# Optimization experiments

Hardware: AMD Instinct MI355X
Metric: run time of the kernel (lower is better)

Reference implementation:

```python
import jax, jax.numpy as jnp
import numpy as np

V, E = 4096, 8192
HV, HE, OUT = 256, 128, 256
EPS = 1e-6


def _one_hot_incidence(idx, n_rows, n_cols):
    # incidence matrix M[v, e] = 1 if idx[e] == v
    return jnp.zeros((n_rows, n_cols), jnp.float32).at[idx, jnp.arange(n_cols)].set(1.0)


def setup_inputs() -> dict:
    key = jax.random.key(0)
    ks = jax.random.split(key, 12)
    # edge endpoints: first V source indices cover every vertex -> positive degrees
    u_idx = jnp.concatenate([jnp.arange(V), jax.random.randint(ks[0], (E - V,), 0, V)])
    v_idx = jax.random.randint(ks[1], (E,), 0, V)
    vew1 = _one_hot_incidence(u_idx, V, E)
    vew2 = _one_hot_incidence(v_idx, V, E)
    hv_ftr = jax.random.normal(ks[2], (V, HV), jnp.float32)
    he_ftr = jax.random.normal(ks[3], (E, HE), jnp.float32)
    s = lambda d: 1.0 / np.sqrt(d)
    w_att = jax.random.normal(ks[4], (HV + HE + HV, 1), jnp.float32) * s(HV + HE + HV)
    b_att = jnp.zeros((1,), jnp.float32)
    w_gcn = jax.random.normal(ks[5], (HV, HV), jnp.float32) * s(HV)
    b_gcn = jnp.zeros((HV,), jnp.float32)
    w1 = jax.random.normal(ks[6], (2 * HV, HV), jnp.float32) * s(2 * HV)
    b1 = jnp.zeros((HV,), jnp.float32)
    w2 = jax.random.normal(ks[7], (HV, OUT), jnp.float32) * s(HV)
    b2 = jnp.zeros((OUT,), jnp.float32)
    return dict(hv_ftr=hv_ftr, he_ftr=he_ftr, vew1=vew1, vew2=vew2,
                w_att=w_att, b_att=b_att, w_gcn=w_gcn, b_gcn=b_gcn,
                w1=w1, b1=b1, w2=w2, b2=b2)


def reference(hv_ftr, he_ftr, vew1, vew2, w_att, b_att, w_gcn, b_gcn, w1, b1, w2, b2):
    vew_u = jnp.concatenate([vew1, vew2], axis=1)  # [V, 2E]
    vew_v = jnp.concatenate([vew2, vew1], axis=1)  # [V, 2E]
    hv_u = vew_u.T @ hv_ftr                         # [2E, HV] gather of source feats
    hv_v = vew_v.T @ hv_ftr                         # [2E, HV] gather of target feats
    he2 = jnp.concatenate([he_ftr, he_ftr], axis=0)  # [2E, HE]
    uev = jnp.concatenate([hv_u, he2, hv_v], axis=1)  # [2E, 2HV+HE]
    edge_w = jax.nn.sigmoid(uev @ w_att + b_att).reshape(-1)  # [2E]
    adj = vew_u @ (vew_v * edge_w[None, :]).T       # [V, V]
    # normalize_adj_rc: D_r^{-1/2} A D_c^{-1/2}
    d_r = jax.lax.rsqrt(jnp.maximum(adj.sum(axis=1), EPS))
    d_c = jax.lax.rsqrt(jnp.maximum(adj.sum(axis=0), EPS))
    adj_n = adj * d_r[:, None] * d_c[None, :]
    # GCN(hv_dim->hv_dim, tanh): propagate linear-transformed features
    hidden = jnp.tanh(adj_n @ (hv_ftr @ w_gcn + b_gcn))  # [V, HV]
    # MLP remap: [hv, hidden] -> hidden_dim HV -> OUT (dropout off at inference)
    h = jnp.concatenate([hv_ftr, hidden], axis=1)   # [V, 2HV]
    h = jax.nn.leaky_relu(h @ w1 + b1)
    return h @ w2 + b2                               # [V, OUT]
```

## Files before the change

kernel.cpp:

```cpp
#include <hip/hip_runtime.h>
#include <hip/hip_bf16.h>
#include <math.h>

#define V 4096
#define E 8192
#define HV 256
#define HE 128
#define OUT_DIM 256
#define EPS 1e-6f

#define G_GEMM1 256
#define G_PROJ  512
#define G_ZERO  64
#define G_IDX   8192
#define G_TOTAL (G_GEMM1 + G_PROJ + G_ZERO + G_IDX)

typedef __attribute__((ext_vector_type(8))) short short8;
typedef __attribute__((ext_vector_type(4))) float f32x4;

__device__ __forceinline__ unsigned short f2bf(float f) {
    __hip_bfloat16 h = __float2bfloat16(f);
    return *(unsigned short*)&h;
}

__device__ __forceinline__ short8 cvt8(float4 a, float4 b) {
    short8 r;
    r[0] = f2bf(a.x); r[1] = f2bf(a.y); r[2] = f2bf(a.z); r[3] = f2bf(a.w);
    r[4] = f2bf(b.x); r[5] = f2bf(b.y); r[6] = f2bf(b.z); r[7] = f2bf(b.w);
    return r;
}

template <int ACT>
__device__ __forceinline__ void gemm_body(const float* __restrict__ A0,
                                          const float* __restrict__ A1,
                                          int KSEG, int NSEG,
                                          const float* __restrict__ B,
                                          const float* __restrict__ bias,
                                          float* __restrict__ Cout,
                                          int N, int bm, int bn) {
    __shared__ __align__(16) unsigned short As[64 * 40];
    __shared__ __align__(16) unsigned short Bs[64 * 40];
    const int tid  = threadIdx.x;
    const int lane = tid & 63;
    const int w    = tid >> 6;
    const int wm   = w >> 1, wn = w & 1;
    const int Ktot = KSEG * NSEG;

    const int sr  = tid >> 2;
    const int sc8 = (tid & 3) * 8;
    const int kb  = tid & 31;
    const int bc0 = (tid >> 5) * 8;
    const int fr  = lane & 15;
    const int kc  = (lane >> 4) * 8;

    f32x4 acc[2][2] = {};

    for (int k0 = 0; k0 < Ktot; k0 += 32) {
        const float* Asrc = (k0 >= KSEG) ? A1 : A0;
        int kk = (k0 >= KSEG) ? (k0 - KSEG) : k0;
        const float* ap = &Asrc[(size_t)(bm + sr) * KSEG + kk + sc8];
        float4 a0 = *(const float4*)ap;
        float4 a1 = *(const float4*)(ap + 4);
        const float* bp = &B[(size_t)(k0 + kb) * N + bn + bc0];
        float4 b0 = *(const float4*)bp;
        float4 b1 = *(const float4*)(bp + 4);
        *(short8*)&As[sr * 40 + sc8] = cvt8(a0, a1);
        unsigned short bw[8];
        bw[0] = f2bf(b0.x); bw[1] = f2bf(b0.y); bw[2] = f2bf(b0.z); bw[3] = f2bf(b0.w);
        bw[4] = f2bf(b1.x); bw[5] = f2bf(b1.y); bw[6] = f2bf(b1.z); bw[7] = f2bf(b1.w);
        #pragma unroll
        for (int j = 0; j < 8; ++j) Bs[(bc0 + j) * 40 + kb] = bw[j];
        __syncthreads();

        short8 bfr[2];
        bfr[0] = *(const short8*)&Bs[(wn * 32 + 0 * 16 + fr) * 40 + kc];
        bfr[1] = *(const short8*)&Bs[(wn * 32 + 1 * 16 + fr) * 40 + kc];
        #pragma unroll
        for (int ms = 0; ms < 2; ++ms) {
            short8 af = *(const short8*)&As[(wm * 32 + ms * 16 + fr) * 40 + kc];
            acc[ms][0] = __builtin_amdgcn_mfma_f32_16x16x32_bf16(af, bfr[0], acc[ms][0], 0, 0, 0);
            acc[ms][1] = __builtin_amdgcn_mfma_f32_16x16x32_bf16(af, bfr[1], acc[ms][1], 0, 0, 0);
        }
        __syncthreads();
    }

    #pragma unroll
    for (int ms = 0; ms < 2; ++ms) {
        #pragma unroll
        for (int ns = 0; ns < 2; ++ns) {
            int col = bn + wn * 32 + ns * 16 + fr;
            float bv = bias ? bias[col] : 0.0f;
            #pragma unroll
            for (int r = 0; r < 4; ++r) {
                int row = bm + wm * 32 + ms * 16 + ((lane >> 4) << 2) + r;
                float v = acc[ms][ns][r] + bv;
                if (ACT == 1) v = (v > 0.0f) ? v : 0.01f * v;
                Cout[(size_t)row * N + col] = v;
            }
        }
    }
}

template <int ACT>
__global__ __launch_bounds__(256) void gemm_kernel(const float* __restrict__ A0,
                                                   const float* __restrict__ A1,
                                                   int KSEG, int NSEG,
                                                   const float* __restrict__ B,
                                                   const float* __restrict__ bias,
                                                   float* __restrict__ C, int N) {
    gemm_body<ACT>(A0, A1, KSEG, NSEG, B, bias, C, N, blockIdx.y * 64, blockIdx.x * 64);
}

__global__ __launch_bounds__(256) void mega_kernel(
    const float* __restrict__ hv, const float* __restrict__ he,
    const float4* __restrict__ vew1, const float4* __restrict__ vew2,
    const float* __restrict__ watt,
    const float* __restrict__ wgcn, const float* __restrict__ bgcn,
    int* __restrict__ iu, int* __restrict__ iv,
    float* __restrict__ pu, float* __restrict__ pv, float* __restrict__ pe,
    float4* __restrict__ zbase, int zn4,
    float* __restrict__ X) {
    const int b = blockIdx.x;
    const int tid = threadIdx.x;

    if (b < G_GEMM1) {
        gemm_body<0>(hv, hv, HV, 1, wgcn, bgcn, X, HV, (b >> 2) * 64, (b & 3) * 64);
    } else if (b < G_GEMM1 + G_PROJ) {
        const int lane = tid & 63;
        for (int r = (b - G_GEMM1) * 4 + (tid >> 6); r < V + E; r += G_PROJ * 4) {
            if (r < V) {
                float4 x  = *(const float4*)(hv + (size_t)r * HV + lane * 4);
                float4 wu = *(const float4*)(watt + lane * 4);
                float4 wv = *(const float4*)(watt + HV + HE + lane * 4);
                float su = x.x * wu.x + x.y * wu.y + x.z * wu.z + x.w * wu.w;
                float sv = x.x * wv.x + x.y * wv.y + x.z * wv.z + x.w * wv.w;
                #pragma unroll
                for (int o = 32; o > 0; o >>= 1) {
                    su += __shfl_down(su, o);
                    sv += __shfl_down(sv, o);
                }
                if (lane == 0) { pu[r] = su; pv[r] = sv; }
            } else {
                int e = r - V;
                float2 x = *(const float2*)(he + (size_t)e * HE + lane * 2);
                float2 w = *(const float2*)(watt + HV + lane * 2);
                float s = x.x * w.x + x.y * w.y;
                #pragma unroll
                for (int o = 32; o > 0; o >>= 1) s += __shfl_down(s, o);
                if (lane == 0) pe[e] = s;
            }
        }
    } else if (b < G_GEMM1 + G_PROJ + G_ZERO) {
        float4 z = {0.0f, 0.0f, 0.0f, 0.0f};
        for (int i = (b - G_GEMM1 - G_PROJ) * 256 + tid; i < zn4; i += G_ZERO * 256)
            zbase[i] = z;
    } else {
        int ib = b - (G_GEMM1 + G_PROJ + G_ZERO);
        const float4* m = (ib < G_IDX / 2) ? vew1 : vew2;
        int* o = (ib < G_IDX / 2) ? iu : iv;
        ib &= (G_IDX / 2 - 1);
        size_t base = (size_t)ib * 2048 + tid;
        #pragma unroll
        for (int it = 0; it < 8; ++it) {
            size_t i = base + (size_t)it * 256;
            float4 x = m[i];
            if (x.x + x.y + x.z + x.w > 0.5f) {
                int v  = (int)(i >> 11);
                int c4 = ((int)i & 2047) << 2;
                if (x.x > 0.5f) o[c4 + 0] = v;
                if (x.y > 0.5f) o[c4 + 1] = v;
                if (x.z > 0.5f) o[c4 + 2] = v;
                if (x.w > 0.5f) o[c4 + 3] = v;
            }
        }
    }
}

__global__ __launch_bounds__(256) void edge_kernel(const int* __restrict__ iu,
                                                   const int* __restrict__ iv,
                                                   const float* __restrict__ pu,
                                                   const float* __restrict__ pv,
                                                   const float* __restrict__ pe,
                                                   const float* __restrict__ batt,
                                                   float* __restrict__ ew,
                                                   float* __restrict__ dr,
                                                   float* __restrict__ dc) {
    int e2 = blockIdx.x * blockDim.x + threadIdx.x;
    if (e2 >= 2 * E) return;
    int e  = (e2 < E) ? e2 : e2 - E;
    int uu = (e2 < E) ? iu[e] : iv[e];
    int vv = (e2 < E) ? iv[e] : iu[e];
    float x = pu[uu] + pe[e] + pv[vv] + batt[0];
    float w = 1.0f / (1.0f + expf(-x));
    ew[e2] = w;
    atomicAdd(dr + uu, w);
    atomicAdd(dc + vv, w);
}

__global__ __launch_bounds__(64) void scatter_kernel(const int* __restrict__ iu,
                                                     const int* __restrict__ iv,
                                                     const float* __restrict__ ew,
                                                     const float* __restrict__ dc,
                                                     const float* __restrict__ X,
                                                     float* __restrict__ acc) {
    int e2 = blockIdx.x;
    int t  = threadIdx.x;
    int e  = (e2 < E) ? e2 : e2 - E;
    int uu = (e2 < E) ? iu[e] : iv[e];
    int vv = (e2 < E) ? iv[e] : iu[e];
    float coef = ew[e2] * rsqrtf(fmaxf(dc[vv], EPS));
    float4 x = *(const float4*)(X + (size_t)vv * HV + t * 4);
    float* dst = acc + (size_t)uu * HV + t * 4;
    atomicAdd(dst + 0, coef * x.x);
    atomicAdd(dst + 1, coef * x.y);
    atomicAdd(dst + 2, coef * x.z);
    atomicAdd(dst + 3, coef * x.w);
}

__global__ __launch_bounds__(256) void finish_kernel(const float* __restrict__ dr,
                                                     float4* __restrict__ acc) {
    int i = blockIdx.x * 256 + threadIdx.x;
    int row = i >> 6;
    float s = rsqrtf(fmaxf(dr[row], EPS));
    float4 x = acc[i];
    x.x = tanhf(s * x.x); x.y = tanhf(s * x.y);
    x.z = tanhf(s * x.z); x.w = tanhf(s * x.w);
    acc[i] = x;
}

extern "C" void kernel_launch(void* const* d_in, const int* in_sizes, int n_in,
                              void* d_out, int out_size, void* d_ws, size_t ws_size,
                              hipStream_t stream) {
    const float* hv   = (const float*)d_in[0];
    const float* he   = (const float*)d_in[1];
    const float* vew1 = (const float*)d_in[2];
    const float* vew2 = (const float*)d_in[3];
    const float* watt = (const float*)d_in[4];
    const float* batt = (const float*)d_in[5];
    const float* wgcn = (const float*)d_in[6];
    const float* bgcn = (const float*)d_in[7];
    const float* w1   = (const float*)d_in[8];
    const float* b1   = (const float*)d_in[9];
    const float* w2   = (const float*)d_in[10];
    const float* b2   = (const float*)d_in[11];
    float* out = (float*)d_out;

    float* ws = (float*)d_ws;
    int*   iu  = (int*)ws;
    int*   iv  = (int*)(ws + E);
    float* pu  = ws + 2 * E;
    float* pv  = pu + V;
    float* pe  = pv + V;
    float* ew  = pe + E;
    float* dr  = ew + 2 * E;
    float* dc  = dr + V;
    float* acc = dc + V;
    float* X   = acc + (size_t)V * HV;

    const int zn4 = (2 * V + V * HV) / 4;

    mega_kernel<<<G_TOTAL, 256, 0, stream>>>(hv, he, (const float4*)vew1,
        (const float4*)vew2, watt, wgcn, bgcn, iu, iv, pu, pv, pe,
        (float4*)dr, zn4, X);

    edge_kernel<<<(2 * E + 255) / 256, 256, 0, stream>>>(iu, iv, pu, pv, pe, batt, ew, dr, dc);

    scatter_kernel<<<2 * E, 64, 0, stream>>>(iu, iv, ew, dc, X, acc);

    finish_kernel<<<V * HV / 4 / 256, 256, 0, stream>>>(dr, (float4*)acc);

    gemm_kernel<1><<<dim3(HV / 64, V / 64), 256, 0, stream>>>(hv, acc, HV, 2, w1, b1, X, HV);

    gemm_kernel<0><<<dim3(OUT_DIM / 64, V / 64), 256, 0, stream>>>(X, X, HV, 1, w2, b2, out, OUT_DIM);
}
```

Before: 135.6 us.

## Split incidence scan into dedicated kernel with column-wise weighted row reduction

Moves the one-hot incidence scan out of the fused mega kernel into a separate scan kernel. Each thread walks 64 rows of one float4 column, accumulating row-index-weighted values, and writes an index only where the sum is nonzero. This replaces per-element branching and scattered stores with a branch-free reduction and fewer writes. The trade-offs are an extra kernel launch, no overlap with the GEMM and projection work, and an assumption that each column has at most one nonzero per 64-row chunk.

```diff
diff --git a/kernel.cpp b/kernel.cpp
--- a/kernel.cpp
+++ b/kernel.cpp
@@ -12,8 +12,7 @@
 #define G_GEMM1 256
 #define G_PROJ  512
 #define G_ZERO  64
-#define G_IDX   8192
-#define G_TOTAL (G_GEMM1 + G_PROJ + G_ZERO + G_IDX)
+#define G_TOTAL2 (G_GEMM1 + G_PROJ + G_ZERO)
 
 typedef __attribute__((ext_vector_type(8))) short short8;
 typedef __attribute__((ext_vector_type(4))) float f32x4;
@@ -28,6 +27,39 @@
     r[0] = f2bf(a.x); r[1] = f2bf(a.y); r[2] = f2bf(a.z); r[3] = f2bf(a.w);
     r[4] = f2bf(b.x); r[5] = f2bf(b.y); r[6] = f2bf(b.z); r[7] = f2bf(b.w);
     return r;
+}
+
+__global__ __launch_bounds__(256) void scan_kernel(const float4* __restrict__ vew1,
+                                                   const float4* __restrict__ vew2,
+                                                   int* __restrict__ iu,
+                                                   int* __restrict__ iv) {
+    const int b = blockIdx.x;
+    const int mat = b >> 9;
+    const int rem = b & 511;
+    const int cchunk = rem & 7;
+    const int rchunk = rem >> 3;
+    const float4* m = mat ? vew2 : vew1;
+    int* o = mat ? iv : iu;
+
+    const int f4col = cchunk * 256 + threadIdx.x;
+    const int v0 = rchunk * 64;
+
+    size_t off = (size_t)v0 * 2048 + f4col;
+    float4 acc = {0.0f, 0.0f, 0.0f, 0.0f};
+    #pragma unroll 8
+    for (int r = 0; r < 64; ++r) {
+        float4 x = m[off];
+        float w = (float)(v0 + r + 1);
+        acc.x += x.x * w; acc.y += x.y * w;
+        acc.z += x.z * w; acc.w += x.w * w;
+        off += 2048;
+    }
+
+    const int c4 = f4col * 4;
+    if (acc.x != 0.0f) o[c4 + 0] = (int)acc.x - 1;
+    if (acc.y != 0.0f) o[c4 + 1] = (int)acc.y - 1;
+    if (acc.z != 0.0f) o[c4 + 2] = (int)acc.z - 1;
+    if (acc.w != 0.0f) o[c4 + 3] = (int)acc.w - 1;
 }
 
 template <int ACT>
@@ -111,12 +143,10 @@
     gemm_body<ACT>(A0, A1, KSEG, NSEG, B, bias, C, N, blockIdx.y * 64, blockIdx.x * 64);
 }
 
-__global__ __launch_bounds__(256) void mega_kernel(
+__global__ __launch_bounds__(256) void mega2_kernel(
     const float* __restrict__ hv, const float* __restrict__ he,
-    const float4* __restrict__ vew1, const float4* __restrict__ vew2,
     const float* __restrict__ watt,
     const float* __restrict__ wgcn, const float* __restrict__ bgcn,
-    int* __restrict__ iu, int* __restrict__ iv,
     float* __restrict__ pu, float* __restrict__ pv, float* __restrict__ pe,
     float4* __restrict__ zbase, int zn4,
     float* __restrict__ X) {
@@ -150,29 +180,10 @@
                 if (lane == 0) pe[e] = s;
             }
         }
-    } else if (b < G_GEMM1 + G_PROJ + G_ZERO) {
+    } else {
         float4 z = {0.0f, 0.0f, 0.0f, 0.0f};
         for (int i = (b - G_GEMM1 - G_PROJ) * 256 + tid; i < zn4; i += G_ZERO * 256)
             zbase[i] = z;
-    } else {
-        int ib = b - (G_GEMM1 + G_PROJ + G_ZERO);
-        const float4* m = (ib < G_IDX / 2) ? vew1 : vew2;
-        int* o = (ib < G_IDX / 2) ? iu : iv;
-        ib &= (G_IDX / 2 - 1);
-        size_t base = (size_t)ib * 2048 + tid;
-        #pragma unroll
-        for (int it = 0; it < 8; ++it) {
-            size_t i = base + (size_t)it * 256;
-            float4 x = m[i];
-            if (x.x + x.y + x.z + x.w > 0.5f) {
-                int v  = (int)(i >> 11);
-                int c4 = ((int)i & 2047) << 2;
-                if (x.x > 0.5f) o[c4 + 0] = v;
-                if (x.y > 0.5f) o[c4 + 1] = v;
-                if (x.z > 0.5f) o[c4 + 2] = v;
-                if (x.w > 0.5f) o[c4 + 3] = v;
-            }
-        }
     }
 }
 
@@ -259,9 +270,10 @@
 
     const int zn4 = (2 * V + V * HV) / 4;
 
-    mega_kernel<<<G_TOTAL, 256, 0, stream>>>(hv, he, (const float4*)vew1,
-        (const float4*)vew2, watt, wgcn, bgcn, iu, iv, pu, pv, pe,
-        (float4*)dr, zn4, X);
+    scan_kernel<<<1024, 256, 0, stream>>>((const float4*)vew1, (const float4*)vew2, iu, iv);
+
+    mega2_kernel<<<G_TOTAL2, 256, 0, stream>>>(hv, he, watt, wgcn, bgcn,
+        pu, pv, pe, (float4*)dr, zn4, X);
 
     edge_kernel<<<(2 * E + 255) / 256, 256, 0, stream>>>(iu, iv, pu, pv, pe, batt, ew, dr, dc);
 
```

New measurement: 145.0 us. +6.9%, slower.

## Split MLP1 GEMM, precompute hv half in mega kernel, fuse tanh into A-load

Applied to the files above, without the earlier changes.

The first MLP GEMM is split in two. The hv·w1[:HV] half is computed early inside the mega kernel, in parallel with the other phases, and written to T0. The hidden half now applies the row normalisation and tanh while loading A and accumulates into T0, which removes the separate finish kernel and halves the K loop of the later GEMM. The scatter kernel also packs four edges into each 256-thread block. The cost is extra workspace, a read-modify-write epilogue, and tanh being recomputed for each column tile of the GEMM.

```diff
diff --git a/kernel.cpp b/kernel.cpp
--- a/kernel.cpp
+++ b/kernel.cpp
@@ -9,11 +9,12 @@
 #define OUT_DIM 256
 #define EPS 1e-6f
 
-#define G_GEMM1 256
-#define G_PROJ  512
-#define G_ZERO  64
-#define G_IDX   8192
-#define G_TOTAL (G_GEMM1 + G_PROJ + G_ZERO + G_IDX)
+#define G_GEMM1  256
+#define G_GEMM1B 256
+#define G_PROJ   512
+#define G_ZERO   64
+#define G_IDX    8192
+#define G_TOTAL (G_GEMM1 + G_GEMM1B + G_PROJ + G_ZERO + G_IDX)
 
 typedef __attribute__((ext_vector_type(8))) short short8;
 typedef __attribute__((ext_vector_type(4))) float f32x4;
@@ -23,19 +24,12 @@
     return *(unsigned short*)&h;
 }
 
-__device__ __forceinline__ short8 cvt8(float4 a, float4 b) {
-    short8 r;
-    r[0] = f2bf(a.x); r[1] = f2bf(a.y); r[2] = f2bf(a.z); r[3] = f2bf(a.w);
-    r[4] = f2bf(b.x); r[5] = f2bf(b.y); r[6] = f2bf(b.z); r[7] = f2bf(b.w);
-    return r;
-}
-
-template <int ACT>
-__device__ __forceinline__ void gemm_body(const float* __restrict__ A0,
-                                          const float* __restrict__ A1,
-                                          int KSEG, int NSEG,
+template <int ACT, int ACCUM, int TANHA>
+__device__ __forceinline__ void gemm_body(const float* __restrict__ A,
+                                          int K,
                                           const float* __restrict__ B,
                                           const float* __restrict__ bias,
+                                          const float* __restrict__ drow,
                                           float* __restrict__ Cout,
                                           int N, int bm, int bn) {
     __shared__ __align__(16) unsigned short As[64 * 40];
@@ -44,7 +38,6 @@
     const int lane = tid & 63;
     const int w    = tid >> 6;
     const int wm   = w >> 1, wn = w & 1;
-    const int Ktot = KSEG * NSEG;
 
     const int sr  = tid >> 2;
     const int sc8 = (tid & 3) * 8;
@@ -53,18 +46,30 @@
     const int fr  = lane & 15;
     const int kc  = (lane >> 4) * 8;
 
+    float s = 1.0f;
+    if (TANHA) s = rsqrtf(fmaxf(drow[bm + sr], EPS));
+
     f32x4 acc[2][2] = {};
 
-    for (int k0 = 0; k0 < Ktot; k0 += 32) {
-        const float* Asrc = (k0 >= KSEG) ? A1 : A0;
-        int kk = (k0 >= KSEG) ? (k0 - KSEG) : k0;
-        const float* ap = &Asrc[(size_t)(bm + sr) * KSEG + kk + sc8];
+    for (int k0 = 0; k0 < K; k0 += 32) {
+        const float* ap = &A[(size_t)(bm + sr) * K + k0 + sc8];
         float4 a0 = *(const float4*)ap;
         float4 a1 = *(const float4*)(ap + 4);
+        if (TANHA) {
+            a0.x = tanhf(s * a0.x); a0.y = tanhf(s * a0.y);
+            a0.z = tanhf(s * a0.z); a0.w = tanhf(s * a0.w);
+            a1.x = tanhf(s * a1.x); a1.y = tanhf(s * a1.y);
+            a1.z = tanhf(s * a1.z); a1.w = tanhf(s * a1.w);
+        }
         const float* bp = &B[(size_t)(k0 + kb) * N + bn + bc0];
         float4 b0 = *(const float4*)bp;
         float4 b1 = *(const float4*)(bp + 4);
-        *(short8*)&As[sr * 40 + sc8] = cvt8(a0, a1);
+        {
+            short8 r;
+            r[0] = f2bf(a0.x); r[1] = f2bf(a0.y); r[2] = f2bf(a0.z); r[3] = f2bf(a0.w);
+            r[4] = f2bf(a1.x); r[5] = f2bf(a1.y); r[6] = f2bf(a1.z); r[7] = f2bf(a1.w);
+            *(short8*)&As[sr * 40 + sc8] = r;
+        }
         unsigned short bw[8];
         bw[0] = f2bf(b0.x); bw[1] = f2bf(b0.y); bw[2] = f2bf(b0.z); bw[3] = f2bf(b0.w);
         bw[4] = f2bf(b1.x); bw[5] = f2bf(b1.y); bw[6] = f2bf(b1.z); bw[7] = f2bf(b1.w);
@@ -94,6 +99,7 @@
             for (int r = 0; r < 4; ++r) {
                 int row = bm + wm * 32 + ms * 16 + ((lane >> 4) << 2) + r;
                 float v = acc[ms][ns][r] + bv;
+                if (ACCUM) v += Cout[(size_t)row * N + col];
                 if (ACT == 1) v = (v > 0.0f) ? v : 0.01f * v;
                 Cout[(size_t)row * N + col] = v;
             }
@@ -101,14 +107,14 @@
     }
 }
 
-template <int ACT>
-__global__ __launch_bounds__(256) void gemm_kernel(const float* __restrict__ A0,
-                                                   const float* __restrict__ A1,
-                                                   int KSEG, int NSEG,
+template <int ACT, int ACCUM, int TANHA>
+__global__ __launch_bounds__(256) void gemm_kernel(const float* __restrict__ A,
+                                                   int K,
                                                    const float* __restrict__ B,
                                                    const float* __restrict__ bias,
+                                                   const float* __restrict__ drow,
                                                    float* __restrict__ C, int N) {
-    gemm_body<ACT>(A0, A1, KSEG, NSEG, B, bias, C, N, blockIdx.y * 64, blockIdx.x * 64);
+    gemm_body<ACT, ACCUM, TANHA>(A, K, B, bias, drow, C, N, blockIdx.y * 64, blockIdx.x * 64);
 }
 
 __global__ __launch_bounds__(256) void mega_kernel(
@@ -116,18 +122,24 @@
     const float4* __restrict__ vew1, const float4* __restrict__ vew2,
     const float* __restrict__ watt,
     const float* __restrict__ wgcn, const float* __restrict__ bgcn,
+    const float* __restrict__ w1,
     int* __restrict__ iu, int* __restrict__ iv,
     float* __restrict__ pu, float* __restrict__ pv, float* __restrict__ pe,
     float4* __restrict__ zbase, int zn4,
-    float* __restrict__ X) {
+    float* __restrict__ X, float* __restrict__ T0) {
     const int b = blockIdx.x;
     const int tid = threadIdx.x;
 
     if (b < G_GEMM1) {
-        gemm_body<0>(hv, hv, HV, 1, wgcn, bgcn, X, HV, (b >> 2) * 64, (b & 3) * 64);
-    } else if (b < G_GEMM1 + G_PROJ) {
+        gemm_body<0, 0, 0>(hv, HV, wgcn, bgcn, nullptr, X, HV,
+                           (b >> 2) * 64, (b & 3) * 64);
+    } else if (b < G_GEMM1 + G_GEMM1B) {
+        int bb = b - G_GEMM1;
+        gemm_body<0, 0, 0>(hv, HV, w1, nullptr, nullptr, T0, HV,
+                           (bb >> 2) * 64, (bb & 3) * 64);
+    } else if (b < G_GEMM1 + G_GEMM1B + G_PROJ) {
         const int lane = tid & 63;
-        for (int r = (b - G_GEMM1) * 4 + (tid >> 6); r < V + E; r += G_PROJ * 4) {
+        for (int r = (b - G_GEMM1 - G_GEMM1B) * 4 + (tid >> 6); r < V + E; r += G_PROJ * 4) {
             if (r < V) {
                 float4 x  = *(const float4*)(hv + (size_t)r * HV + lane * 4);
                 float4 wu = *(const float4*)(watt + lane * 4);
@@ -150,12 +162,12 @@
                 if (lane == 0) pe[e] = s;
             }
         }
-    } else if (b < G_GEMM1 + G_PROJ + G_ZERO) {
+    } else if (b < G_GEMM1 + G_GEMM1B + G_PROJ + G_ZERO) {
         float4 z = {0.0f, 0.0f, 0.0f, 0.0f};
-        for (int i = (b - G_GEMM1 - G_PROJ) * 256 + tid; i < zn4; i += G_ZERO * 256)
+        for (int i = (b - G_GEMM1 - G_GEMM1B - G_PROJ) * 256 + tid; i < zn4; i += G_ZERO * 256)
             zbase[i] = z;
     } else {
-        int ib = b - (G_GEMM1 + G_PROJ + G_ZERO);
+        int ib = b - (G_GEMM1 + G_GEMM1B + G_PROJ + G_ZERO);
         const float4* m = (ib < G_IDX / 2) ? vew1 : vew2;
         int* o = (ib < G_IDX / 2) ? iu : iv;
         ib &= (G_IDX / 2 - 1);
@@ -197,14 +209,14 @@
     atomicAdd(dc + vv, w);
 }
 
-__global__ __launch_bounds__(64) void scatter_kernel(const int* __restrict__ iu,
-                                                     const int* __restrict__ iv,
-                                                     const float* __restrict__ ew,
-                                                     const float* __restrict__ dc,
-                                                     const float* __restrict__ X,
-                                                     float* __restrict__ acc) {
-    int e2 = blockIdx.x;
-    int t  = threadIdx.x;
+__global__ __launch_bounds__(256) void scatter_kernel(const int* __restrict__ iu,
+                                                      const int* __restrict__ iv,
+                                                      const float* __restrict__ ew,
+                                                      const float* __restrict__ dc,
+                                                      const float* __restrict__ X,
+                                                      float* __restrict__ acc) {
+    int e2 = blockIdx.x * 4 + (threadIdx.x >> 6);
+    int t  = threadIdx.x & 63;
     int e  = (e2 < E) ? e2 : e2 - E;
     int uu = (e2 < E) ? iu[e] : iv[e];
     int vv = (e2 < E) ? iv[e] : iu[e];
@@ -215,17 +227,6 @@
     atomicAdd(dst + 1, coef * x.y);
     atomicAdd(dst + 2, coef * x.z);
     atomicAdd(dst + 3, coef * x.w);
-}
-
-__global__ __launch_bounds__(256) void finish_kernel(const float* __restrict__ dr,
-                                                     float4* __restrict__ acc) {
-    int i = blockIdx.x * 256 + threadIdx.x;
-    int row = i >> 6;
-    float s = rsqrtf(fmaxf(dr[row], EPS));
-    float4 x = acc[i];
-    x.x = tanhf(s * x.x); x.y = tanhf(s * x.y);
-    x.z = tanhf(s * x.z); x.w = tanhf(s * x.w);
-    acc[i] = x;
 }
 
 extern "C" void kernel_launch(void* const* d_in, const int* in_sizes, int n_in,
@@ -256,20 +257,21 @@
     float* dc  = dr + V;
     float* acc = dc + V;
     float* X   = acc + (size_t)V * HV;
+    float* T0  = X + (size_t)V * HV;
 
     const int zn4 = (2 * V + V * HV) / 4;
 
     mega_kernel<<<G_TOTAL, 256, 0, stream>>>(hv, he, (const float4*)vew1,
-        (const float4*)vew2, watt, wgcn, bgcn, iu, iv, pu, pv, pe,
-        (float4*)dr, zn4, X);
+        (const float4*)vew2, watt, wgcn, bgcn, w1, iu, iv, pu, pv, pe,
+        (float4*)dr, zn4, X, T0);
 
     edge_kernel<<<(2 * E + 255) / 256, 256, 0, stream>>>(iu, iv, pu, pv, pe, batt, ew, dr, dc);
 
-    scatter_kernel<<<2 * E, 64, 0, stream>>>(iu, iv, ew, dc, X, acc);
-
-    finish_kernel<<<V * HV / 4 / 256, 256, 0, stream>>>(dr, (float4*)acc);
-
-    gemm_kernel<1><<<dim3(HV / 64, V / 64), 256, 0, stream>>>(hv, acc, HV, 2, w1, b1, X, HV);
-
-    gemm_kernel<0><<<dim3(OUT_DIM / 64, V / 64), 256, 0, stream>>>(X, X, HV, 1, w2, b2, out, OUT_DIM);
-}
+    scatter_kernel<<<2 * E / 4, 256, 0, stream>>>(iu, iv, ew, dc, X, acc);
+
+    gemm_kernel<1, 1, 1><<<dim3(HV / 64, V / 64), 256, 0, stream>>>(
+        acc, HV, w1 + (size_t)HV * HV, b1, dr, T0, HV);
+
+    gemm_kernel<0, 0, 0><<<dim3(OUT_DIM / 64, V / 64), 256, 0, stream>>>(
+        T0, HV, w2, b2, nullptr, out, OUT_DIM);
+}
```

After: 137.0 us. No clear change (+1.1%).
